# Kernel optimization log

Hardware: AMD Instinct MI355X
Metric: run time of the kernel (lower is better)

Reference implementation:

```python
import jax, jax.numpy as jnp
import numpy as np

N_NODES = 100000
N_EDGES = 1600000
HID = 128
NODE_C = 128
PRED_C = 64


def setup_inputs() -> dict:
    key = jax.random.key(0)
    ks = jax.random.split(key, 9)
    s = 1.0 / np.sqrt(HID)
    sn = 1.0 / np.sqrt(NODE_C)
    return {
        "x": jax.random.normal(ks[0], (N_NODES, HID), dtype=jnp.float32),
        "u": jax.random.normal(ks[1], (N_NODES, NODE_C), dtype=jnp.float32),
        "edge_index": jax.random.randint(ks[2], (2, N_EDGES), 0, N_NODES, dtype=jnp.int64),
        "W_w": jax.random.uniform(ks[3], (HID, HID), jnp.float32, -s, s),
        "W_b": jax.random.uniform(ks[4], (HID,), jnp.float32, -s, s),
        "phi_w": jax.random.uniform(ks[5], (HID, NODE_C), jnp.float32, -sn, sn),
        "phi_b": jax.random.uniform(ks[6], (HID,), jnp.float32, -sn, sn),
        "pred_w": jax.random.uniform(ks[7], (PRED_C, HID), jnp.float32, -s, s),
        "pred_b": jax.random.uniform(ks[8], (PRED_C,), jnp.float32, -s, s),
    }


def reference(x, u, edge_index, W_w, W_b, phi_w, phi_b, pred_w, pred_b):
    src, tgt = edge_index[0], edge_index[1]
    # x <- W(x): [N, HID]
    h = x @ W_w.T + W_b
    # message = h[src]; aggregate = scatter-sum at tgt
    msg = h[src]  # [E, HID]
    agg = jax.ops.segment_sum(msg, tgt, num_segments=x.shape[0])  # [N, HID]
    # update: agg + phi(u), then activation
    x_new = jax.nn.relu(agg + u @ phi_w.T + phi_b)
    # prediction head
    y = x_new @ pred_w.T + pred_b
    return (x_new, y)
```

## Files before the change

### kernel.cpp

```cpp
#include <hip/hip_runtime.h>

#define NN 100000
#define NE 1600000
#define HD 128
#define NB 391
#define CAP 64
#define EPB 4096

typedef __attribute__((ext_vector_type(8))) short short8;
typedef __attribute__((ext_vector_type(4))) float v4f;
union U8 { uint4 u; short8 s; };

__device__ inline unsigned pk2(float a, float b) {
  unsigned ua = __float_as_uint(a), ub = __float_as_uint(b);
  ua = (ua + 0x7fffu + ((ua >> 16) & 1u)) >> 16;
  ub = (ub + 0x7fffu + ((ub >> 16) & 1u)) >> 16;
  return ua | (ub << 16);
}
__device__ inline float blo(unsigned h) { return __uint_as_float(h << 16); }
__device__ inline float bhi(unsigned h) { return __uint_as_float(h & 0xffff0000u); }

__global__ __launch_bounds__(256) void cvt_bf16(
    const float* __restrict__ src, unsigned short* __restrict__ dst, int n8)
{
  int i = blockIdx.x * 256 + threadIdx.x;
  if (i >= n8) return;
  const float4* s = (const float4*)src + (size_t)i * 2;
  float4 a = s[0], b = s[1];
  uint4 o;
  o.x = pk2(a.x, a.y); o.y = pk2(a.z, a.w);
  o.z = pk2(b.x, b.y); o.w = pk2(b.z, b.w);
  ((uint4*)dst)[i] = o;
}

__global__ __launch_bounds__(256) void cvt_weights(
    const float* __restrict__ W, const float* __restrict__ phi,
    const float* __restrict__ pred,
    unsigned short* __restrict__ Wb, unsigned short* __restrict__ phib,
    unsigned short* __restrict__ predb)
{
  int i = blockIdx.x * 256 + threadIdx.x;
  if (i >= 5120) return;
  const float* s; unsigned short* d; int j;
  if (i < 2048)      { s = W;    d = Wb;    j = i; }
  else if (i < 4096) { s = phi;  d = phib;  j = i - 2048; }
  else               { s = pred; d = predb; j = i - 4096; }
  const float4* sp = (const float4*)s + (size_t)j * 2;
  float4 a = sp[0], b = sp[1];
  uint4 o;
  o.x = pk2(a.x, a.y); o.y = pk2(a.z, a.w);
  o.z = pk2(b.x, b.y); o.w = pk2(b.z, b.w);
  ((uint4*)d)[j] = o;
}

__global__ __launch_bounds__(512) void k_zero(unsigned* __restrict__ meta) {
  int t = threadIdx.x;
  if (t < NB) meta[t] = 0;
  if (t == 0) meta[1536] = 0;
}

__global__ __launch_bounds__(512) void k_hist(
    const int* __restrict__ ei, unsigned* __restrict__ meta)
{
  __shared__ unsigned lh[NB];
  const int t = threadIdx.x;
  for (int i = t; i < NB; i += 512) lh[i] = 0;
  __syncthreads();
#pragma unroll
  for (int j = 0; j < 8; j++) {
    int e = blockIdx.x * EPB + j * 512 + t;
    if (e < NE) {
      unsigned tgt = (unsigned)ei[NE + e];
      atomicAdd(&lh[tgt >> 8], 1u);
    }
  }
  __syncthreads();
  for (int i = t; i < NB; i += 512)
    if (lh[i]) atomicAdd(&meta[i], lh[i]);
}

__global__ __launch_bounds__(512) void k_scan(unsigned* __restrict__ meta) {
  __shared__ unsigned sc[512];
  const int t = threadIdx.x;
  unsigned v = (t < NB) ? meta[t] : 0u;
  sc[t] = v;
  for (int off = 1; off < 512; off <<= 1) {
    __syncthreads();
    unsigned w = (t >= off) ? sc[t - off] : 0u;
    __syncthreads();
    sc[t] += w;
  }
  unsigned excl = sc[t] - v;
  if (t < NB) { meta[512 + t] = excl; meta[1024 + t] = excl; }
}

__global__ __launch_bounds__(512) void k_part(
    const int* __restrict__ ei, unsigned* __restrict__ meta,
    unsigned* __restrict__ edge_part)
{
  __shared__ unsigned lh[512], sc[512], lb[512], gb[512], lcur[512];
  __shared__ unsigned staged[EPB], sgo[EPB];
  __shared__ unsigned tot;
  const int t = threadIdx.x;
  lh[t] = 0;
  __syncthreads();

  unsigned rec[8]; short bb[8];
#pragma unroll
  for (int j = 0; j < 8; j++) {
    int e = blockIdx.x * EPB + j * 512 + t;
    if (e < NE) {
      unsigned tgt = (unsigned)ei[NE + e];
      unsigned src = (unsigned)ei[e];
      unsigned b = tgt >> 8;
      rec[j] = ((tgt & 255u) << 17) | src;
      bb[j] = (short)b;
      atomicAdd(&lh[b], 1u);
    } else bb[j] = -1;
  }
  __syncthreads();

  unsigned v = lh[t];
  sc[t] = v;
  for (int off = 1; off < 512; off <<= 1) {
    __syncthreads();
    unsigned w = (t >= off) ? sc[t - off] : 0u;
    __syncthreads();
    sc[t] += w;
  }
  lb[t] = sc[t] - v;
  lcur[t] = lb[t];
  if (t == 511) tot = sc[511];
  gb[t] = (t < NB && v) ? atomicAdd(&meta[1024 + t], v) : 0u;
  __syncthreads();

#pragma unroll
  for (int j = 0; j < 8; j++) {
    if (bb[j] >= 0) {
      unsigned b = (unsigned)bb[j];
      unsigned o = atomicAdd(&lcur[b], 1u);
      staged[o] = rec[j];
      sgo[o] = gb[b] + (o - lb[b]);
    }
  }
  __syncthreads();
  unsigned T = tot;
#pragma unroll
  for (int j = 0; j < 8; j++) {
    unsigned idx = j * 512 + t;
    if (idx < T) edge_part[sgo[idx]] = staged[idx];
  }
}

__global__ __launch_bounds__(512) void k_gather(
    const unsigned* __restrict__ edge_part, const unsigned* __restrict__ meta,
    const unsigned* __restrict__ xbu,
    unsigned* __restrict__ aggbu,
    float* __restrict__ degf,
    unsigned* __restrict__ oflw, unsigned* __restrict__ meta_oflw)
{
  __shared__ unsigned cnt[256];
  __shared__ unsigned list[256 * CAP];
  const int t = threadIdx.x;
  const unsigned b = blockIdx.x;
  const unsigned nbase = b << 8;
  const unsigned ebase = meta[512 + b];
  const unsigned ecnt  = meta[b];
  if (t < 256) cnt[t] = 0;
  __syncthreads();

  for (unsigned k = t; k < ecnt; k += 512) {
    unsigned rec = edge_part[ebase + k];
    unsigned tl = rec >> 17;
    unsigned src = rec & 0x1FFFFu;
    unsigned p = atomicAdd(&cnt[tl], 1u);
    if (p < CAP) list[tl * CAP + p] = src;
    else {
      unsigned op = atomicAdd(&meta_oflw[1536], 1u);
      oflw[op * 2] = nbase + tl;
      oflw[op * 2 + 1] = src;
    }
  }
  __syncthreads();

  const int wave = t >> 6, lane = t & 63;
  for (int k = 0; k < 32; k++) {
    unsigned tl = wave * 32 + k;
    long n = (long)nbase + tl;
    if (n >= NN) continue;
    unsigned deg = cnt[tl];
    if (lane == 0) degf[n] = (float)deg;
    int d2 = deg < CAP ? (int)deg : CAP;
    int my = (lane < d2) ? (int)list[tl * CAP + lane] : 0;
    float ax = 0.f, ay = 0.f;
    int e = 0;
    for (; e + 2 <= d2; e += 2) {
      int s0 = __shfl(my, e, 64);
      int s1 = __shfl(my, e + 1, 64);
      unsigned h0 = xbu[(size_t)s0 * 64 + lane];
      unsigned h1 = xbu[(size_t)s1 * 64 + lane];
      ax += blo(h0); ay += bhi(h0);
      ax += blo(h1); ay += bhi(h1);
    }
    if (e < d2) {
      int s0 = __shfl(my, e, 64);
      unsigned h0 = xbu[(size_t)s0 * 64 + lane];
      ax += blo(h0); ay += bhi(h0);
    }
    aggbu[n * 64 + lane] = pk2(ax, ay);
  }
}

__global__ __launch_bounds__(64) void k_oflow(
    const unsigned* __restrict__ meta, const unsigned* __restrict__ oflw,
    const float* __restrict__ x, unsigned* __restrict__ aggbu)
{
  const int t = threadIdx.x;
  unsigned m = meta[1536];
  for (unsigned i = 0; i < m; i++) {
    unsigned tgt = oflw[i * 2], src = oflw[i * 2 + 1];
    unsigned c = aggbu[(size_t)tgt * 64 + t];
    float a0 = blo(c) + x[(size_t)src * HD + t * 2];
    float a1 = bhi(c) + x[(size_t)src * HD + t * 2 + 1];
    aggbu[(size_t)tgt * 64 + t] = pk2(a0, a1);
  }
}

__global__ __launch_bounds__(256) void k_fused(
    const unsigned* __restrict__ aggbu,
    const float* __restrict__ u,
    const float* __restrict__ degf,
    const unsigned short* __restrict__ Wb,
    const unsigned short* __restrict__ phib,
    const unsigned short* __restrict__ predb,
    const float* __restrict__ W_b, const float* __restrict__ phi_b,
    const float* __restrict__ pred_b,
    float* __restrict__ out_x, float* __restrict__ out_y)
{
  __shared__ unsigned xs[4 * 32 * 64];
  const int lane = threadIdx.x & 63;
  const int wv   = threadIdx.x >> 6;
  const long n0  = (long)blockIdx.x * 128 + wv * 32;
  const int r = lane & 15, h4 = lane >> 4;

  U8 xf[2][4], uf[2][4];
  float dg[2];
#pragma unroll
  for (int nt = 0; nt < 2; nt++) {
    long n = n0 + nt * 16 + r;
    long nc = (n < NN) ? n : 0;
    dg[nt] = degf[nc];
    const unsigned* arow = aggbu + nc * 64 + h4 * 4;
    const float* urow = u + nc * HD + h4 * 8;
#pragma unroll
    for (int ks = 0; ks < 4; ks++) {
      xf[nt][ks].u = *(const uint4*)(arow + ks * 16);
      float4 a = *(const float4*)(urow + ks * 32);
      float4 b = *(const float4*)(urow + ks * 32 + 4);
      uf[nt][ks].u = make_uint4(pk2(a.x, a.y), pk2(a.z, a.w),
                                pk2(b.x, b.y), pk2(b.z, b.w));
    }
  }

#pragma unroll
  for (int ct = 0; ct < 8; ct++) {
    const int c0 = ct * 16 + r;
    float4 wb4 = *(const float4*)&W_b[ct * 16 + h4 * 4];
    float4 pb4 = *(const float4*)&phi_b[ct * 16 + h4 * 4];
    v4f acc[2];
#pragma unroll
    for (int nt = 0; nt < 2; nt++)
      acc[nt] = (v4f){fmaf(dg[nt], wb4.x, pb4.x), fmaf(dg[nt], wb4.y, pb4.y),
                      fmaf(dg[nt], wb4.z, pb4.z), fmaf(dg[nt], wb4.w, pb4.w)};
#pragma unroll
    for (int ks = 0; ks < 4; ks++) {
      short8 wf = *(const short8*)&Wb[(size_t)c0 * HD + ks * 32 + h4 * 8];
      acc[0] = __builtin_amdgcn_mfma_f32_16x16x32_bf16(wf, xf[0][ks].s, acc[0], 0, 0, 0);
      acc[1] = __builtin_amdgcn_mfma_f32_16x16x32_bf16(wf, xf[1][ks].s, acc[1], 0, 0, 0);
    }
#pragma unroll
    for (int ks = 0; ks < 4; ks++) {
      short8 pf = *(const short8*)&phib[(size_t)c0 * HD + ks * 32 + h4 * 8];
      acc[0] = __builtin_amdgcn_mfma_f32_16x16x32_bf16(pf, uf[0][ks].s, acc[0], 0, 0, 0);
      acc[1] = __builtin_amdgcn_mfma_f32_16x16x32_bf16(pf, uf[1][ks].s, acc[1], 0, 0, 0);
    }
#pragma unroll
    for (int nt = 0; nt < 2; nt++) {
      float r0 = fmaxf(acc[nt][0], 0.f), r1 = fmaxf(acc[nt][1], 0.f);
      float r2 = fmaxf(acc[nt][2], 0.f), r3 = fmaxf(acc[nt][3], 0.f);
      long n = n0 + nt * 16 + r;
      if (n < NN)
        *(float4*)&out_x[n * HD + ct * 16 + h4 * 4] = make_float4(r0, r1, r2, r3);
      int lr = nt * 16 + r;
      int chunk = ct * 2 + (h4 >> 1);
      unsigned* dst = &xs[(wv * 32 + lr) * 64 + ((chunk ^ r) << 2) + ((h4 & 1) << 1)];
      *(uint2*)dst = make_uint2(pk2(r0, r1), pk2(r2, r3));
    }
  }
  __syncthreads();

#pragma unroll
  for (int ct2 = 0; ct2 < 4; ct2++) {
    float4 qb4 = *(const float4*)&pred_b[ct2 * 16 + h4 * 4];
    v4f acc[2];
    acc[0] = (v4f){qb4.x, qb4.y, qb4.z, qb4.w};
    acc[1] = acc[0];
#pragma unroll
    for (int ks = 0; ks < 4; ks++) {
      short8 pw = *(const short8*)&predb[(size_t)(ct2 * 16 + r) * HD + ks * 32 + h4 * 8];
#pragma unroll
      for (int nt = 0; nt < 2; nt++) {
        U8 bx;
        bx.u = *(const uint4*)&xs[(wv * 32 + nt * 16 + r) * 64 + (((h4 + ks * 4) ^ r) << 2)];
        acc[nt] = __builtin_amdgcn_mfma_f32_16x16x32_bf16(pw, bx.s, acc[nt], 0, 0, 0);
      }
    }
#pragma unroll
    for (int nt = 0; nt < 2; nt++) {
      long n = n0 + nt * 16 + r;
      if (n < NN)
        *(float4*)&out_y[n * 64 + ct2 * 16 + h4 * 4] =
            make_float4(acc[nt][0], acc[nt][1], acc[nt][2], acc[nt][3]);
    }
  }
}

template<int CT, int LDO, bool RELU_WB>
__global__ __launch_bounds__(256) void gemm_nodes(
    const float* __restrict__ in, float* in_wb,
    const float* __restrict__ Wg, const float* __restrict__ bias,
    float* __restrict__ out)
{
  __shared__ float Wt[HD * CT];
  __shared__ float xsh[32 * HD];
  const int tid = threadIdx.x;
  const int cbase = blockIdx.y * CT;
  for (int idx = tid; idx < HD * CT; idx += 256) {
    int c = idx >> 7, k = idx & 127;
    int chunk = ((c >> 1) ^ (k & 31));
    Wt[k * CT + (chunk << 1 | (c & 1))] = Wg[(size_t)(cbase + c) * HD + k];
  }
  const long nb = (long)blockIdx.x * 32;
  for (int idx = tid; idx < 32 * HD; idx += 256) {
    int n = idx >> 7, k = idx & 127;
    float v = in[(nb + n) * HD + k];
    if (RELU_WB) { v = fmaxf(v, 0.0f); in_wb[(nb + n) * HD + k] = v; }
    xsh[idx] = v;
  }
  __syncthreads();
  const int lane = tid & 31, grp = tid >> 5, c0 = lane * 2;
  float acc[4][2];
#pragma unroll
  for (int j = 0; j < 4; j++) { acc[j][0] = bias[cbase + c0]; acc[j][1] = bias[cbase + c0 + 1]; }
#pragma unroll 4
  for (int k = 0; k < HD; k += 4) {
    float xv[4][4];
#pragma unroll
    for (int j = 0; j < 4; j++) {
      float4 t = *(const float4*)&xsh[(grp * 4 + j) * HD + k];
      xv[j][0] = t.x; xv[j][1] = t.y; xv[j][2] = t.z; xv[j][3] = t.w;
    }
#pragma unroll
    for (int kk = 0; kk < 4; kk++) {
      int chunk = lane ^ ((k + kk) & 31);
      float2 w = *(const float2*)&Wt[(k + kk) * CT + (chunk << 1)];
#pragma unroll
      for (int j = 0; j < 4; j++) {
        acc[j][0] = fmaf(xv[j][kk], w.x, acc[j][0]);
        acc[j][1] = fmaf(xv[j][kk], w.y, acc[j][1]);
      }
    }
  }
#pragma unroll
  for (int j = 0; j < 4; j++) {
    long n = nb + grp * 4 + j;
    *(float2*)&out[n * LDO + c0 + cbase] = make_float2(acc[j][0], acc[j][1]);
  }
}

__global__ __launch_bounds__(256) void scatter_edges(
    const int* __restrict__ ei, const float* __restrict__ h, float* __restrict__ agg)
{
  const long t = (long)blockIdx.x * 256 + threadIdx.x;
  const int e = (int)(t >> 5), lane = (int)(t & 31);
  const int src = ei[e], tgt = ei[NE + e];
  const float4 v = *(const float4*)&h[(size_t)src * HD + lane * 4];
  float* dst = &agg[(size_t)tgt * HD + lane * 4];
  unsafeAtomicAdd(dst + 0, v.x); unsafeAtomicAdd(dst + 1, v.y);
  unsafeAtomicAdd(dst + 2, v.z); unsafeAtomicAdd(dst + 3, v.w);
}

extern "C" void kernel_launch(void* const* d_in, const int* in_sizes, int n_in,
                              void* d_out, int out_size, void* d_ws, size_t ws_size,
                              hipStream_t stream) {
  const float* x      = (const float*)d_in[0];
  const float* u      = (const float*)d_in[1];
  const int*   ei     = (const int*)d_in[2];
  const float* W_w    = (const float*)d_in[3];
  const float* W_b    = (const float*)d_in[4];
  const float* phi_w  = (const float*)d_in[5];
  const float* phi_b  = (const float*)d_in[6];
  const float* pred_w = (const float*)d_in[7];
  const float* pred_b = (const float*)d_in[8];

  float* out_x = (float*)d_out;
  float* out_y = (float*)d_out + (size_t)NN * HD;

  char* p = (char*)d_ws;
  auto take = [&](size_t bytes) { char* r = p; p += (bytes + 255) & ~(size_t)255; return r; };
  unsigned short* xb  = (unsigned short*)take((size_t)NN * HD * 2);
  unsigned* aggbu     = (unsigned*)take((size_t)NN * 64 * 4);
  unsigned* edge_part = (unsigned*)take((size_t)NE * 4);
  unsigned* oflw      = (unsigned*)take((size_t)NE * 8);
  float* degf         = (float*)take((size_t)NN * 4);
  unsigned short* Wb    = (unsigned short*)take(16384 * 2);
  unsigned short* phib  = (unsigned short*)take(16384 * 2);
  unsigned short* predb = (unsigned short*)take(8192 * 2);
  unsigned* meta      = (unsigned*)take(2048 * 4);
  const size_t need = (size_t)(p - (char*)d_ws);

  dim3 b256(256), b512(512);
  if (ws_size >= need) {
    const int n8x = NN * HD / 8;
    cvt_bf16<<<dim3((n8x + 255) / 256), b256, 0, stream>>>(x, xb, n8x);
    cvt_weights<<<dim3(20), b256, 0, stream>>>(W_w, phi_w, pred_w, Wb, phib, predb);
    k_zero<<<dim3(1), b512, 0, stream>>>(meta);
    k_hist<<<dim3((NE + EPB - 1) / EPB), b512, 0, stream>>>(ei, meta);
    k_scan<<<dim3(1), b512, 0, stream>>>(meta);
    k_part<<<dim3((NE + EPB - 1) / EPB), b512, 0, stream>>>(ei, meta, edge_part);
    k_gather<<<dim3(NB), b512, 0, stream>>>(edge_part, meta, (const unsigned*)xb,
                                            aggbu, degf, oflw, meta);
    k_oflow<<<dim3(1), dim3(64), 0, stream>>>(meta, oflw, x, aggbu);
    k_fused<<<dim3((NN + 127) / 128), b256, 0, stream>>>(
        aggbu, u, degf, Wb, phib, predb, W_b, phi_b, pred_b, out_x, out_y);
  } else {
    float* h = (float*)d_ws;
    gemm_nodes<64, 128, false><<<dim3(NN / 32, 2), b256, 0, stream>>>(x, nullptr, W_w, W_b, h);
    gemm_nodes<64, 128, false><<<dim3(NN / 32, 2), b256, 0, stream>>>(u, nullptr, phi_w, phi_b, out_x);
    scatter_edges<<<dim3((NE * 32) / 256), b256, 0, stream>>>(ei, h, out_x);
    gemm_nodes<64, 64, true><<<dim3(NN / 32, 1), b256, 0, stream>>>(out_x, out_x, pred_w, pred_b, out_y);
  }
}
```

Measured before the change: 375.4 us.

## Split gather into quarter-bucket blocks with 16-byte row loads and merge zero kernel

The gather kernel now launches four blocks per 256-node bucket. Each block filters the bucket's edges down to its own 64 nodes, which increases parallelism and cuts LDS use. Inside a wave, the edges of a node are processed four at a time by 16-lane groups, each loading a full 256-byte bf16 row with uint4 loads, and the partial sums are combined with xor shuffles. The separate zeroing kernel is folded into an extra block of the weight conversion kernel, removing one launch. In exchange, each block reads the whole bucket's edge list, so edge-list reads are four times redundant.

```diff
diff --git a/kernel.cpp b/kernel.cpp
--- a/kernel.cpp
+++ b/kernel.cpp
@@ -4,6 +4,7 @@
 #define NE 1600000
 #define HD 128
 #define NB 391
+#define QN 64
 #define CAP 64
 #define EPB 4096
 
@@ -37,10 +38,14 @@
     const float* __restrict__ W, const float* __restrict__ phi,
     const float* __restrict__ pred,
     unsigned short* __restrict__ Wb, unsigned short* __restrict__ phib,
-    unsigned short* __restrict__ predb)
-{
+    unsigned short* __restrict__ predb, unsigned* __restrict__ meta)
+{
+  if (blockIdx.x == 20) {
+    for (int j = threadIdx.x; j < NB; j += 256) meta[j] = 0;
+    if (threadIdx.x == 0) meta[1536] = 0;
+    return;
+  }
   int i = blockIdx.x * 256 + threadIdx.x;
-  if (i >= 5120) return;
   const float* s; unsigned short* d; int j;
   if (i < 2048)      { s = W;    d = Wb;    j = i; }
   else if (i < 4096) { s = phi;  d = phib;  j = i - 2048; }
@@ -53,12 +58,6 @@
   ((uint4*)d)[j] = o;
 }
 
-__global__ __launch_bounds__(512) void k_zero(unsigned* __restrict__ meta) {
-  int t = threadIdx.x;
-  if (t < NB) meta[t] = 0;
-  if (t == 0) meta[1536] = 0;
-}
-
 __global__ __launch_bounds__(512) void k_hist(
     const int* __restrict__ ei, unsigned* __restrict__ meta)
 {
@@ -154,60 +153,68 @@
 
 __global__ __launch_bounds__(512) void k_gather(
     const unsigned* __restrict__ edge_part, const unsigned* __restrict__ meta,
-    const unsigned* __restrict__ xbu,
+    const uint4* __restrict__ xb4,
     unsigned* __restrict__ aggbu,
     float* __restrict__ degf,
     unsigned* __restrict__ oflw, unsigned* __restrict__ meta_oflw)
 {
-  __shared__ unsigned cnt[256];
-  __shared__ unsigned list[256 * CAP];
+  __shared__ unsigned cnt[QN];
+  __shared__ unsigned list[QN * CAP];
   const int t = threadIdx.x;
-  const unsigned b = blockIdx.x;
-  const unsigned nbase = b << 8;
+  const unsigned b = blockIdx.x >> 2;
+  const unsigned q = blockIdx.x & 3;
+  const unsigned nbase = (b << 8) + (q << 6);
   const unsigned ebase = meta[512 + b];
   const unsigned ecnt  = meta[b];
-  if (t < 256) cnt[t] = 0;
+  if (t < QN) cnt[t] = 0;
   __syncthreads();
 
   for (unsigned k = t; k < ecnt; k += 512) {
     unsigned rec = edge_part[ebase + k];
     unsigned tl = rec >> 17;
-    unsigned src = rec & 0x1FFFFu;
-    unsigned p = atomicAdd(&cnt[tl], 1u);
-    if (p < CAP) list[tl * CAP + p] = src;
-    else {
-      unsigned op = atomicAdd(&meta_oflw[1536], 1u);
-      oflw[op * 2] = nbase + tl;
-      oflw[op * 2 + 1] = src;
+    if ((tl >> 6) == q) {
+      unsigned ql = tl & 63;
+      unsigned src = rec & 0x1FFFFu;
+      unsigned p = atomicAdd(&cnt[ql], 1u);
+      if (p < CAP) list[ql * CAP + p] = src;
+      else {
+        unsigned op = atomicAdd(&meta_oflw[1536], 1u);
+        oflw[op * 2] = nbase + ql;
+        oflw[op * 2 + 1] = src;
+      }
     }
   }
   __syncthreads();
 
   const int wave = t >> 6, lane = t & 63;
-  for (int k = 0; k < 32; k++) {
-    unsigned tl = wave * 32 + k;
-    long n = (long)nbase + tl;
+  const int g = lane >> 4, c = lane & 15;
+#pragma unroll
+  for (int k = 0; k < 8; k++) {
+    unsigned ql = wave * 8 + k;
+    long n = (long)nbase + ql;
     if (n >= NN) continue;
-    unsigned deg = cnt[tl];
+    unsigned deg = cnt[ql];
     if (lane == 0) degf[n] = (float)deg;
     int d2 = deg < CAP ? (int)deg : CAP;
-    int my = (lane < d2) ? (int)list[tl * CAP + lane] : 0;
-    float ax = 0.f, ay = 0.f;
-    int e = 0;
-    for (; e + 2 <= d2; e += 2) {
-      int s0 = __shfl(my, e, 64);
-      int s1 = __shfl(my, e + 1, 64);
-      unsigned h0 = xbu[(size_t)s0 * 64 + lane];
-      unsigned h1 = xbu[(size_t)s1 * 64 + lane];
-      ax += blo(h0); ay += bhi(h0);
-      ax += blo(h1); ay += bhi(h1);
-    }
-    if (e < d2) {
-      int s0 = __shfl(my, e, 64);
-      unsigned h0 = xbu[(size_t)s0 * 64 + lane];
-      ax += blo(h0); ay += bhi(h0);
-    }
-    aggbu[n * 64 + lane] = pk2(ax, ay);
+    float a[8] = {0, 0, 0, 0, 0, 0, 0, 0};
+    for (int e = g; e < d2; e += 4) {
+      unsigned s = list[ql * CAP + e];
+      uint4 v = xb4[(size_t)s * 16 + c];
+      a[0] += blo(v.x); a[1] += bhi(v.x);
+      a[2] += blo(v.y); a[3] += bhi(v.y);
+      a[4] += blo(v.z); a[5] += bhi(v.z);
+      a[6] += blo(v.w); a[7] += bhi(v.w);
+    }
+#pragma unroll
+    for (int m = 16; m <= 32; m <<= 1)
+#pragma unroll
+      for (int j = 0; j < 8; j++)
+        a[j] += __shfl_xor(a[j], m, 64);
+    if (g == 0) {
+      uint4 o = make_uint4(pk2(a[0], a[1]), pk2(a[2], a[3]),
+                           pk2(a[4], a[5]), pk2(a[6], a[7]));
+      *(uint4*)&aggbu[n * 64 + c * 4] = o;
+    }
   }
 }
 
@@ -423,13 +430,12 @@
   if (ws_size >= need) {
     const int n8x = NN * HD / 8;
     cvt_bf16<<<dim3((n8x + 255) / 256), b256, 0, stream>>>(x, xb, n8x);
-    cvt_weights<<<dim3(20), b256, 0, stream>>>(W_w, phi_w, pred_w, Wb, phib, predb);
-    k_zero<<<dim3(1), b512, 0, stream>>>(meta);
+    cvt_weights<<<dim3(21), b256, 0, stream>>>(W_w, phi_w, pred_w, Wb, phib, predb, meta);
     k_hist<<<dim3((NE + EPB - 1) / EPB), b512, 0, stream>>>(ei, meta);
     k_scan<<<dim3(1), b512, 0, stream>>>(meta);
     k_part<<<dim3((NE + EPB - 1) / EPB), b512, 0, stream>>>(ei, meta, edge_part);
-    k_gather<<<dim3(NB), b512, 0, stream>>>(edge_part, meta, (const unsigned*)xb,
-                                            aggbu, degf, oflw, meta);
+    k_gather<<<dim3(NB * 4), b512, 0, stream>>>(edge_part, meta, (const uint4*)xb,
+                                                aggbu, degf, oflw, meta);
     k_oflow<<<dim3(1), dim3(64), 0, stream>>>(meta, oflw, x, aggbu);
     k_fused<<<dim3((NN + 127) / 128), b256, 0, stream>>>(
         aggbu, u, degf, Wb, phib, predb, W_b, phi_b, pred_b, out_x, out_y);
```

After: 318.8 us. -15.1%, faster.
